# Kernel tuning notes

Hardware: AMD Instinct MI355X
Metric: run time of the kernel (lower is better)

Reference implementation:

```python
import jax, jax.numpy as jnp
import numpy as np

GS = 128          # r_group_size
Q_MAX = 7.0       # 2**(q_bits-1)-1, q_bits=4
R_MAX = 7.0       # 2**(r_bits-1)-1, r_bits=4
R_MIN = -8.0      # -R_MAX-1
EPS = 1e-8


def _fake_quant_group(w, n_bits=4, group_size=128, eps=1e-8):
    # symmetric group-wise fake quant of the weight (done once at __init__)
    qmax = 2 ** (n_bits - 1) - 1
    qmin = -qmax - 1
    O, I = w.shape
    wg = w.reshape(O, I // group_size, group_size)
    scale = jnp.maximum(jnp.max(jnp.abs(wg), axis=-1, keepdims=True) / qmax, eps)
    wq = jnp.clip(jnp.round(wg / scale), qmin, qmax) * scale
    return wq.reshape(O, I)


def _select_pow2_base(t):
    # smallest value in {2,4,8,16,32,64} that is >= t (64 if none)
    base = jnp.full_like(t, 64.0)
    for v in (32.0, 16.0, 8.0, 4.0, 2.0):
        base = jnp.where(t <= v, jnp.full_like(t, v), base)
    return base


def setup_inputs() -> dict:
    key = jax.random.key(0)
    kx, kw, kb = jax.random.split(key, 3)
    B, S, IN, OUT = 4, 2048, 4096, 11008
    x = jax.random.normal(kx, (B, S, IN), dtype=jnp.float32)
    w_raw = jax.random.normal(kw, (OUT, IN), dtype=jnp.float32)
    weight = _fake_quant_group(w_raw, n_bits=4, group_size=128)
    bias = jax.random.normal(kb, (OUT,), dtype=jnp.float32)
    return {"x": x, "weight": weight, "bias": bias}


def reference(x, weight, bias):
    # dynamic quotient-remainder activation fake-quant (init path)
    H = x.shape[-1]
    xg = x.astype(jnp.float32).reshape(x.shape[:-1] + (H // GS, GS))  # [..., G, gs]
    max_abs = jnp.maximum(jnp.max(jnp.abs(xg), axis=-1, keepdims=True), EPS)
    base = _select_pow2_base(max_abs / Q_MAX)                 # [..., G, 1]
    q = jnp.clip(jnp.round(xg / base), -Q_MAX, Q_MAX)          # quotient
    r = xg - base * q                                          # remainder
    max_abs_r = jnp.maximum(jnp.max(jnp.abs(r), axis=-1, keepdims=True), EPS)
    scale_r = max_abs_r / R_MAX
    r_dq = jnp.clip(jnp.round(r / scale_r), R_MIN, R_MAX) * scale_r
    x_recon = (base * q + r_dq).reshape(x.shape)
    # F.linear: y = x @ W^T + b
    return jnp.einsum("bsi,oi->bso", x_recon, weight) + bias
```

## Files before the change

### kernel.cpp

```cpp
#include <hip/hip_runtime.h>
#include <stdint.h>
#include <stddef.h>

typedef __bf16 bf16x8 __attribute__((ext_vector_type(8)));
typedef float  f32x4  __attribute__((ext_vector_type(4)));
typedef float  f32x2  __attribute__((ext_vector_type(2)));

__device__ __forceinline__ unsigned short f2bf(float f) {
  unsigned int u = __builtin_bit_cast(unsigned int, f);
  u += 0x7fffu + ((u >> 16) & 1u);
  return (unsigned short)(u >> 16);
}

__device__ __forceinline__ void gld_lds16(const void* g, void* l) {
  __builtin_amdgcn_global_load_lds(
      (__attribute__((address_space(1))) void*)(g),
      (__attribute__((address_space(3))) void*)(l), 16, 0, 0);
}

#define BAR()     asm volatile("s_barrier" ::: "memory")
#define WAITVM(n) asm volatile("s_waitcnt vmcnt(" #n ")" ::: "memory")

__global__ __launch_bounds__(256) void quant_x_kernel(
    const float* __restrict__ x, unsigned short* __restrict__ xb, long long ngroups)
{
  const int lane = threadIdx.x & 63;
  const int wv   = threadIdx.x >> 6;
  long long g = (long long)blockIdx.x * 4 + wv;
  if (g >= ngroups) return;

  const float* xg = x + g * 128;
  f32x2 v = __builtin_nontemporal_load(
      reinterpret_cast<const f32x2*>(xg + lane * 2));

  float m = fmaxf(fabsf(v[0]), fabsf(v[1]));
  #pragma unroll
  for (int off = 32; off; off >>= 1) m = fmaxf(m, __shfl_xor(m, off));
  m = fmaxf(m, 1e-8f);

  float t = m / 7.0f;
  float base = t <= 2.f ? 2.f : t <= 4.f ? 4.f : t <= 8.f ? 8.f
             : t <= 16.f ? 16.f : t <= 32.f ? 32.f : 64.f;
  float inv_base = 1.0f / base;

  float q0 = fminf(fmaxf(rintf(v[0] * inv_base), -7.f), 7.f);
  float q1 = fminf(fmaxf(rintf(v[1] * inv_base), -7.f), 7.f);
  float r0 = v[0] - base * q0;
  float r1 = v[1] - base * q1;

  float mr = fmaxf(fabsf(r0), fabsf(r1));
  #pragma unroll
  for (int off = 32; off; off >>= 1) mr = fmaxf(mr, __shfl_xor(mr, off));
  mr = fmaxf(mr, 1e-8f);
  float scale_r = mr / 7.0f;

  float rd0 = fminf(fmaxf(rintf(r0 / scale_r), -8.f), 7.f) * scale_r;
  float rd1 = fminf(fmaxf(rintf(r1 / scale_r), -8.f), 7.f) * scale_r;

  float y0 = base * q0 + rd0;
  float y1 = base * q1 + rd1;

  unsigned int packed = (unsigned int)f2bf(y0) | ((unsigned int)f2bf(y1) << 16);
  *reinterpret_cast<unsigned int*>(xb + g * 128 + lane * 2) = packed;
}

__global__ __launch_bounds__(256) void cvt_w_kernel(
    const float* __restrict__ w, unsigned short* __restrict__ wb, long long n)
{
  long long i = ((long long)blockIdx.x * blockDim.x + threadIdx.x) * 8;
  if (i + 7 >= n) {
    if (i >= n) return;
    for (long long j = i; j < n; ++j) wb[j] = f2bf(w[j]);
    return;
  }
  f32x4 v0 = __builtin_nontemporal_load(reinterpret_cast<const f32x4*>(w + i));
  f32x4 v1 = __builtin_nontemporal_load(reinterpret_cast<const f32x4*>(w + i + 4));
  uint4 o;
  o.x = (unsigned)f2bf(v0[0]) | ((unsigned)f2bf(v0[1]) << 16);
  o.y = (unsigned)f2bf(v0[2]) | ((unsigned)f2bf(v0[3]) << 16);
  o.z = (unsigned)f2bf(v1[0]) | ((unsigned)f2bf(v1[1]) << 16);
  o.w = (unsigned)f2bf(v1[2]) | ((unsigned)f2bf(v1[3]) << 16);
  *reinterpret_cast<uint4*>(wb + i) = o;
}

#define BM 256
#define BN 256
#define BK 64

#define MFMA16(a, b, c) __builtin_amdgcn_mfma_f32_16x16x32_bf16(a, b, c, 0, 0, 0)

__global__ __launch_bounds__(512, 2) void gemm256_bias(
    const unsigned short* __restrict__ A,
    const unsigned short* __restrict__ B,
    const float* __restrict__ bias,
    float* __restrict__ C,
    int M, int N, int K)
{
  __shared__ unsigned short lds[2][2][2][128 * 64];

  const int tid  = threadIdx.x;
  const int lane = tid & 63;
  const int wid  = tid >> 6;
  const int wm   = wid >> 2;
  const int wn   = wid & 3;
  const int laneq = lane & 15;
  const int laneh = lane >> 4;
  const int lq7   = laneq & 7;

  const int ntm = M / BM;
  const int ntn = N / BN;
  int tm, tn;
  if ((ntm & 15) == 0) {
    int rem = blockIdx.x;
    int str = 0, stc = 0, w = 16;
    for (;;) {
      int w2 = (ntn - stc * 16 < 16) ? (ntn - stc * 16) : 16;
      int sz = 16 * w2;
      if (rem < sz) { w = w2; break; }
      rem -= sz;
      ++stc;
      if (stc * 16 >= ntn) { stc = 0; ++str; }
    }
    tm = str * 16 + rem / w;
    tn = stc * 16 + rem % w;
  } else {
    tm = (int)blockIdx.x / ntn;
    tn = (int)blockIdx.x % ntn;
  }
  const size_t m0 = (size_t)tm * BM;
  const size_t n0 = (size_t)tn * BN;

  const int NT = K / BK;

  const int s0 = ((0 * 4 + laneh) ^ lq7) * 8;
  const int s1 = ((1 * 4 + laneh) ^ lq7) * 8;

  f32x4 acc[8][4];
  #pragma unroll
  for (int i = 0; i < 8; i++)
    #pragma unroll
    for (int j = 0; j < 4; j++)
      acc[i][j] = (f32x4){0.f, 0.f, 0.f, 0.f};

  auto stage = [&](int mat, int d, int h, int kt) {
    const unsigned short* gbase = (mat == 0)
        ? (A + (m0 + (size_t)h * 128) * (size_t)K)
        : (B + (n0 + (size_t)h * 128) * (size_t)K);
    const int k0 = kt * BK;
    #pragma unroll
    for (int l = 0; l < 2; ++l) {
      int c   = l * 512 + tid;
      int row = c >> 3;
      int s   = (c & 7) ^ (row & 7);
      gld_lds16(gbase + (size_t)row * K + k0 + s * 8,
                (char*)&lds[d][mat][h][0] + (l * 512 + wid * 64) * 16);
    }
  };

  stage(0, 0, 0, 0); stage(0, 0, 1, 0);
  stage(1, 0, 0, 0); stage(1, 0, 1, 0);
  stage(0, 1, 0, 1); stage(0, 1, 1, 1);
  stage(1, 1, 0, 1); stage(1, 1, 1, 1);
  WAITVM(8);
  BAR();

  for (int t = 0; t < NT; ++t) {
    const int d = t & 1;
    const unsigned short* As_ = &lds[d][0][wm][0];
    const unsigned short* Bs_ = &lds[d][1][wn >> 1][0];
    const int brow = (wn & 1) * 64;

    bf16x8 af[4][2], bl[2][2], bh[2][2];

    #pragma unroll
    for (int mi = 0; mi < 4; ++mi) {
      af[mi][0] = *(const bf16x8*)&As_[(mi * 16 + laneq) * 64 + s0];
      af[mi][1] = *(const bf16x8*)&As_[(mi * 16 + laneq) * 64 + s1];
    }
    #pragma unroll
    for (int nj = 0; nj < 2; ++nj) {
      bl[nj][0] = *(const bf16x8*)&Bs_[(brow + nj * 16 + laneq) * 64 + s0];
      bl[nj][1] = *(const bf16x8*)&Bs_[(brow + nj * 16 + laneq) * 64 + s1];
    }
    BAR();
    __builtin_amdgcn_s_setprio(1);
    #pragma unroll
    for (int mi = 0; mi < 4; ++mi)
      #pragma unroll
      for (int nj = 0; nj < 2; ++nj) {
        acc[mi][nj] = MFMA16(af[mi][0], bl[nj][0], acc[mi][nj]);
        acc[mi][nj] = MFMA16(af[mi][1], bl[nj][1], acc[mi][nj]);
      }
    __builtin_amdgcn_s_setprio(0);
    BAR();

    #pragma unroll
    for (int nj = 0; nj < 2; ++nj) {
      bh[nj][0] = *(const bf16x8*)&Bs_[(brow + 32 + nj * 16 + laneq) * 64 + s0];
      bh[nj][1] = *(const bf16x8*)&Bs_[(brow + 32 + nj * 16 + laneq) * 64 + s1];
    }
    BAR();
    __builtin_amdgcn_s_setprio(1);
    #pragma unroll
    for (int mi = 0; mi < 4; ++mi)
      #pragma unroll
      for (int nj = 0; nj < 2; ++nj) {
        acc[mi][2 + nj] = MFMA16(af[mi][0], bh[nj][0], acc[mi][2 + nj]);
        acc[mi][2 + nj] = MFMA16(af[mi][1], bh[nj][1], acc[mi][2 + nj]);
      }
    __builtin_amdgcn_s_setprio(0);
    BAR();

    #pragma unroll
    for (int mi = 0; mi < 4; ++mi) {
      af[mi][0] = *(const bf16x8*)&As_[(64 + mi * 16 + laneq) * 64 + s0];
      af[mi][1] = *(const bf16x8*)&As_[(64 + mi * 16 + laneq) * 64 + s1];
    }
    if (t + 2 < NT) { stage(1, d, 0, t + 2); stage(1, d, 1, t + 2); }
    BAR();
    __builtin_amdgcn_s_setprio(1);
    #pragma unroll
    for (int mi = 0; mi < 4; ++mi)
      #pragma unroll
      for (int nj = 0; nj < 2; ++nj) {
        acc[4 + mi][2 + nj] = MFMA16(af[mi][0], bh[nj][0], acc[4 + mi][2 + nj]);
        acc[4 + mi][2 + nj] = MFMA16(af[mi][1], bh[nj][1], acc[4 + mi][2 + nj]);
      }
    __builtin_amdgcn_s_setprio(0);
    BAR();

    if (t + 2 < NT) { stage(0, d, 0, t + 2); stage(0, d, 1, t + 2); }
    __builtin_amdgcn_s_setprio(1);
    #pragma unroll
    for (int mi = 0; mi < 4; ++mi)
      #pragma unroll
      for (int nj = 0; nj < 2; ++nj) {
        acc[4 + mi][nj] = MFMA16(af[mi][0], bl[nj][0], acc[4 + mi][nj]);
        acc[4 + mi][nj] = MFMA16(af[mi][1], bl[nj][1], acc[4 + mi][nj]);
      }
    __builtin_amdgcn_s_setprio(0);
    if (t == NT - 2)      { WAITVM(0); }
    else if (t < NT - 2)  { WAITVM(8); }
    BAR();
  }

  #pragma unroll
  for (int nj = 0; nj < 4; ++nj) {
    int col = (int)n0 + wn * 64 + nj * 16 + laneq;
    float bv = bias[col];
    #pragma unroll
    for (int mi = 0; mi < 8; ++mi) {
      size_t row = m0 + wm * 128 + mi * 16 + laneh * 4;
      float* cp = C + row * (size_t)N + col;
      #pragma unroll
      for (int r = 0; r < 4; ++r)
        __builtin_nontemporal_store(acc[mi][nj][r] + bv, cp + (size_t)r * N);
    }
  }
}

extern "C" void kernel_launch(void* const* d_in, const int* in_sizes, int n_in,
                              void* d_out, int out_size, void* d_ws, size_t ws_size,
                              hipStream_t stream) {
  const float* x    = (const float*)d_in[0];
  const float* w    = (const float*)d_in[1];
  const float* bias = (const float*)d_in[2];
  float* out = (float*)d_out;

  const long long xN = in_sizes[0];
  const long long wN = in_sizes[1];
  const int N = in_sizes[2];
  const int K = (int)(wN / N);
  const int M = (int)(xN / K);

  unsigned short* xb = (unsigned short*)d_ws;
  unsigned short* wb = xb + xN;

  long long ngroups = xN / 128;
  long long qblocks = (ngroups + 3) / 4;
  quant_x_kernel<<<(int)qblocks, 256, 0, stream>>>(x, xb, ngroups);

  long long cblocks = (wN + 2047) / 2048;
  cvt_w_kernel<<<(int)cblocks, 256, 0, stream>>>(w, wb, wN);

  int grid = (M / BM) * (N / BN);
  gemm256_bias<<<grid, 512, 0, stream>>>(xb, wb, bias, out, M, N, K);
}
```

Before: 805.9 us.

## Replace ping-pong barrier schedule with simple one-ahead double buffering

Restructures the GEMM main loop from a two-tile-ahead prefetch, interleaved with four barrier-separated MFMA phases and setprio hints, into a one-tile-ahead double buffer. Each iteration now issues all loads for the next tile at the top, waits on the current tile, then runs all MFMAs without intermediate barriers. This removes several barriers per iteration and the priority toggling, but shortens the prefetch distance and gives up the explicit wave ping-pong interleaving of loads and compute. It also holds more fragment registers (separate al/ah).

```diff
diff --git a/kernel.cpp b/kernel.cpp
--- a/kernel.cpp
+++ b/kernel.cpp
@@ -159,89 +159,77 @@
 
   stage(0, 0, 0, 0); stage(0, 0, 1, 0);
   stage(1, 0, 0, 0); stage(1, 0, 1, 0);
-  stage(0, 1, 0, 1); stage(0, 1, 1, 1);
-  stage(1, 1, 0, 1); stage(1, 1, 1, 1);
-  WAITVM(8);
-  BAR();
 
   for (int t = 0; t < NT; ++t) {
     const int d = t & 1;
+
+    BAR();
+    if (t + 1 < NT) {
+      const int dn = d ^ 1;
+      stage(0, dn, 0, t + 1); stage(0, dn, 1, t + 1);
+      stage(1, dn, 0, t + 1); stage(1, dn, 1, t + 1);
+      WAITVM(8);
+    } else {
+      WAITVM(0);
+    }
+    BAR();
+
     const unsigned short* As_ = &lds[d][0][wm][0];
     const unsigned short* Bs_ = &lds[d][1][wn >> 1][0];
     const int brow = (wn & 1) * 64;
 
-    bf16x8 af[4][2], bl[2][2], bh[2][2];
+    bf16x8 al[4][2], ah[4][2], bl[2][2], bh[2][2];
 
     #pragma unroll
     for (int mi = 0; mi < 4; ++mi) {
-      af[mi][0] = *(const bf16x8*)&As_[(mi * 16 + laneq) * 64 + s0];
-      af[mi][1] = *(const bf16x8*)&As_[(mi * 16 + laneq) * 64 + s1];
+      al[mi][0] = *(const bf16x8*)&As_[(mi * 16 + laneq) * 64 + s0];
+      al[mi][1] = *(const bf16x8*)&As_[(mi * 16 + laneq) * 64 + s1];
     }
     #pragma unroll
     for (int nj = 0; nj < 2; ++nj) {
       bl[nj][0] = *(const bf16x8*)&Bs_[(brow + nj * 16 + laneq) * 64 + s0];
       bl[nj][1] = *(const bf16x8*)&Bs_[(brow + nj * 16 + laneq) * 64 + s1];
     }
-    BAR();
-    __builtin_amdgcn_s_setprio(1);
-    #pragma unroll
-    for (int mi = 0; mi < 4; ++mi)
-      #pragma unroll
-      for (int nj = 0; nj < 2; ++nj) {
-        acc[mi][nj] = MFMA16(af[mi][0], bl[nj][0], acc[mi][nj]);
-        acc[mi][nj] = MFMA16(af[mi][1], bl[nj][1], acc[mi][nj]);
-      }
-    __builtin_amdgcn_s_setprio(0);
-    BAR();
+    #pragma unroll
+    for (int mi = 0; mi < 4; ++mi)
+      #pragma unroll
+      for (int nj = 0; nj < 2; ++nj) {
+        acc[mi][nj] = MFMA16(al[mi][0], bl[nj][0], acc[mi][nj]);
+        acc[mi][nj] = MFMA16(al[mi][1], bl[nj][1], acc[mi][nj]);
+      }
 
     #pragma unroll
     for (int nj = 0; nj < 2; ++nj) {
       bh[nj][0] = *(const bf16x8*)&Bs_[(brow + 32 + nj * 16 + laneq) * 64 + s0];
       bh[nj][1] = *(const bf16x8*)&Bs_[(brow + 32 + nj * 16 + laneq) * 64 + s1];
     }
-    BAR();
-    __builtin_amdgcn_s_setprio(1);
-    #pragma unroll
-    for (int mi = 0; mi < 4; ++mi)
-      #pragma unroll
-      for (int nj = 0; nj < 2; ++nj) {
-        acc[mi][2 + nj] = MFMA16(af[mi][0], bh[nj][0], acc[mi][2 + nj]);
-        acc[mi][2 + nj] = MFMA16(af[mi][1], bh[nj][1], acc[mi][2 + nj]);
-      }
-    __builtin_amdgcn_s_setprio(0);
-    BAR();
+    #pragma unroll
+    for (int mi = 0; mi < 4; ++mi)
+      #pragma unroll
+      for (int nj = 0; nj < 2; ++nj) {
+        acc[mi][2 + nj] = MFMA16(al[mi][0], bh[nj][0], acc[mi][2 + nj]);
+        acc[mi][2 + nj] = MFMA16(al[mi][1], bh[nj][1], acc[mi][2 + nj]);
+      }
 
     #pragma unroll
     for (int mi = 0; mi < 4; ++mi) {
-      af[mi][0] = *(const bf16x8*)&As_[(64 + mi * 16 + laneq) * 64 + s0];
-      af[mi][1] = *(const bf16x8*)&As_[(64 + mi * 16 + laneq) * 64 + s1];
-    }
-    if (t + 2 < NT) { stage(1, d, 0, t + 2); stage(1, d, 1, t + 2); }
-    BAR();
-    __builtin_amdgcn_s_setprio(1);
-    #pragma unroll
-    for (int mi = 0; mi < 4; ++mi)
-      #pragma unroll
-      for (int nj = 0; nj < 2; ++nj) {
-        acc[4 + mi][2 + nj] = MFMA16(af[mi][0], bh[nj][0], acc[4 + mi][2 + nj]);
-        acc[4 + mi][2 + nj] = MFMA16(af[mi][1], bh[nj][1], acc[4 + mi][2 + nj]);
-      }
-    __builtin_amdgcn_s_setprio(0);
-    BAR();
-
-    if (t + 2 < NT) { stage(0, d, 0, t + 2); stage(0, d, 1, t + 2); }
-    __builtin_amdgcn_s_setprio(1);
-    #pragma unroll
-    for (int mi = 0; mi < 4; ++mi)
-      #pragma unroll
-      for (int nj = 0; nj < 2; ++nj) {
-        acc[4 + mi][nj] = MFMA16(af[mi][0], bl[nj][0], acc[4 + mi][nj]);
-        acc[4 + mi][nj] = MFMA16(af[mi][1], bl[nj][1], acc[4 + mi][nj]);
-      }
-    __builtin_amdgcn_s_setprio(0);
-    if (t == NT - 2)      { WAITVM(0); }
-    else if (t < NT - 2)  { WAITVM(8); }
-    BAR();
+      ah[mi][0] = *(const bf16x8*)&As_[(64 + mi * 16 + laneq) * 64 + s0];
+      ah[mi][1] = *(const bf16x8*)&As_[(64 + mi * 16 + laneq) * 64 + s1];
+    }
+    #pragma unroll
+    for (int mi = 0; mi < 4; ++mi)
+      #pragma unroll
+      for (int nj = 0; nj < 2; ++nj) {
+        acc[4 + mi][2 + nj] = MFMA16(ah[mi][0], bh[nj][0], acc[4 + mi][2 + nj]);
+        acc[4 + mi][2 + nj] = MFMA16(ah[mi][1], bh[nj][1], acc[4 + mi][2 + nj]);
+      }
+    #pragma unroll
+    for (int mi = 0; mi < 4; ++mi)
+      #pragma unroll
+      for (int nj = 0; nj < 2; ++nj) {
+        acc[4 + mi][nj] = MFMA16(ah[mi][0], bl[nj][0], acc[4 + mi][nj]);
+        acc[4 + mi][nj] = MFMA16(ah[mi][1], bl[nj][1], acc[4 + mi][nj]);
+      }
   }
 
   #pragma unroll
```

Measured after the change: 803.4 us. No clear change (-0.3%).
